# Kernel optimization log

Measured on AMD Instinct MI355X. Metric: run time of the kernel, lower is better.

The kernel has to match this reference:

```python
import jax, jax.numpy as jnp
import numpy as np

N_CODE = 1024
D_K = 512
K = 16
BETA = (0.25, 1.0)
N_SMAT = 2
N = 32768


def setup_inputs() -> dict:
    key = jax.random.key(0)
    k1, k2, k3, k4, k5, k6 = jax.random.split(key, 6)
    x = jax.random.normal(k1, (1, N, D_K), dtype=jnp.float32)
    c = jax.random.normal(k2, (N_CODE, D_K), dtype=jnp.float32)
    # trans linears: Linear(n_code, n_code // 2**i) for i = 1..n_smat
    s = 1.0 / np.sqrt(N_CODE)
    W1 = jax.random.uniform(k3, (N_CODE // 2, N_CODE), jnp.float32, -s, s)
    b1 = jax.random.uniform(k4, (N_CODE // 2,), jnp.float32, -s, s)
    W2 = jax.random.uniform(k5, (N_CODE // 4, N_CODE), jnp.float32, -s, s)
    b2 = jax.random.uniform(k6, (N_CODE // 4,), jnp.float32, -s, s)
    return {"x": x, "c": c, "W1": W1, "b1": b1, "W2": W2, "b2": b2,
            "training": 1, "get_k": 0}


def _quantize(x, cb):
    # argmin of squared euclidean distance == argmin of cdist (p=2)
    # d2[n, m] = ||x_n||^2 - 2 x_n . c_m + ||c_m||^2
    d2 = (jnp.sum(x * x, axis=1, keepdims=True)
          - 2.0 * (x @ cb.T)
          + jnp.sum(cb * cb, axis=1))
    z = jnp.argmin(d2, axis=1)
    return z, cb[z]


def _vq_loss(z_q, x):
    # mse(z_q, sg(x)) and mse(x, sg(z_q)); values identical in forward
    e = jnp.mean((z_q - x) ** 2)
    return BETA[0] * e + BETA[1] * e


def reference(x, c, W1, b1, W2, b2, training, get_k):
    x2 = x[0]  # squeeze(0) -> [N, d_k]

    main_z, main_z_q = _quantize(x2, c)

    # sub-scale codebooks: L(c.T).T == W @ c + b[:, None]
    sub_z_q = jnp.zeros_like(main_z_q)
    for W, b in ((W1, b1), (W2, b2)):
        sub_c = W @ c + b[:, None]  # [n_code // 2^i, d_k]
        _, sub_q = _quantize(x2, sub_c)
        sub_z_q = sub_z_q + sub_q
    sub_z_q = sub_z_q / N_SMAT

    if training:
        total_loss = _vq_loss(main_z_q, x2) + _vq_loss(sub_z_q, x2)
    else:
        total_loss = jnp.zeros(())

    # get_k=0 path: ms_k_i stays zeros
    ms_k_i = jnp.zeros((K, D_K), dtype=x2.dtype)

    # unique rows of main_z_q == number of distinct codebook indices used
    counts = jnp.zeros((N_CODE,), jnp.int32).at[main_z].add(1)
    unique_rows = jnp.sum(counts > 0)

    # straight-through (values unchanged in forward)
    main_out = (x2 + jax.lax.stop_gradient(main_z_q - x2))[None]
    sub_out = (x2 + jax.lax.stop_gradient(sub_z_q - x2))[None]
    return main_out, sub_out, total_loss, ms_k_i, unique_rows
```

## Files before the change

### kernel.cpp

```cpp
#include <hip/hip_runtime.h>
#include <cstdint>

typedef unsigned short ushort_t;
typedef unsigned int uint_t;
typedef _Float16 f16x8 __attribute__((ext_vector_type(8)));
typedef float f32x4 __attribute__((ext_vector_type(4)));

#define N_ROWS 32768
#define DK 512
#define NC_MAIN 1024
#define NCB 1792
#define NTILE 14
#define NBLK_RG 8192

#define MAIN_OFF 0
#define SUB_OFF  16777216
#define LOSS_OFF 33554432
#define MSK_OFF  33554433
#define UNIQ_OFF 33562625

__device__ __forceinline__ uint_t umin_(uint_t a, uint_t b) { return a < b ? a : b; }
__device__ __forceinline__ uint_t umax_(uint_t a, uint_t b) { return a > b ? a : b; }

__global__ __launch_bounds__(256) void build_subcb(
    const float* __restrict__ c, const float* __restrict__ W1,
    const float* __restrict__ b1, const float* __restrict__ W2,
    const float* __restrict__ b2, float* __restrict__ CB,
    _Float16* __restrict__ cbh)
{
    int tid = threadIdx.x;
    int tx = tid & 63, ty = tid >> 6;
    int col = blockIdx.x * 64 + tx;
    int row0 = blockIdx.y * 16 + ty * 4;
    if (row0 < 1024) {
#pragma unroll
        for (int r = 0; r < 4; ++r) {
            float v = c[(row0 + r) * DK + col];
            CB[(row0 + r) * DK + col] = v;
            cbh[(row0 + r) * DK + col] = (_Float16)v;
        }
    } else {
        int i0 = row0 - 1024;
        const float* W;
        const float* b;
        if (i0 < 512) { W = W1; b = b1; }
        else          { W = W2; b = b2; i0 -= 512; }
        float acc[4] = {0.f, 0.f, 0.f, 0.f};
#pragma unroll 8
        for (int j = 0; j < 1024; ++j) {
            float cv = c[j * DK + col];
#pragma unroll
            for (int r = 0; r < 4; ++r)
                acc[r] += W[(i0 + r) * 1024 + j] * cv;
        }
#pragma unroll
        for (int r = 0; r < 4; ++r) {
            float v = acc[r] + b[i0 + r];
            CB[(row0 + r) * DK + col] = v;
            cbh[(row0 + r) * DK + col] = (_Float16)v;
        }
    }
}

__global__ __launch_bounds__(64) void row_norms(const float* __restrict__ CB,
                                                float* __restrict__ norms) {
    int row = blockIdx.x;
    int lane = threadIdx.x;
    const float4* p = (const float4*)(CB + (size_t)row * DK);
    float s = 0.f;
#pragma unroll
    for (int i = lane; i < 128; i += 64) {
        float4 v = p[i];
        s += v.x * v.x + v.y * v.y + v.z * v.z + v.w * v.w;
    }
#pragma unroll
    for (int off = 32; off; off >>= 1) s += __shfl_down(s, off, 64);
    if (lane == 0) norms[row] = s;
}

__global__ __launch_bounds__(256) void cvt_x(const float* __restrict__ in,
                                             _Float16* __restrict__ out,
                                             int* __restrict__ used) {
    int i = blockIdx.x * 256 + threadIdx.x;
    if (i < 1024) used[i] = 0;
    const float4* p = (const float4*)in + (size_t)i * 2;
    float4 a = p[0], b = p[1];
    f16x8 o;
    o[0] = (_Float16)a.x; o[1] = (_Float16)a.y; o[2] = (_Float16)a.z; o[3] = (_Float16)a.w;
    o[4] = (_Float16)b.x; o[5] = (_Float16)b.y; o[6] = (_Float16)b.z; o[7] = (_Float16)b.w;
    *((f16x8*)out + i) = o;
}

__device__ __forceinline__ void async16(void* lds, const void* g) {
    __builtin_amdgcn_global_load_lds(
        (const __attribute__((address_space(1))) unsigned int*)(uintptr_t)g,
        (__attribute__((address_space(3))) unsigned int*)(uintptr_t)lds,
        16, 0, 0);
}

__global__ __launch_bounds__(512, 2) void gemm_topk(
    const _Float16* __restrict__ xh, const _Float16* __restrict__ cbh,
    const float* __restrict__ norms, uint2* __restrict__ candbuf)
{
    __shared__ __align__(16) ushort_t As[2][2][256 * 32];
    __shared__ __align__(16) ushort_t Bs[2][2][256 * 32];

    const int tid = threadIdx.x;
    const int lane = tid & 63;
    const int wid = tid >> 6;
    const int wy = wid >> 2, wx = wid & 3;
    const int lane15 = lane & 15, q = lane >> 4;

    const int bid = blockIdx.x;
    const int xcd = bid & 7;
    const int slot = bid >> 3;
    const int tileP = slot % 7;
    const int rowG = slot / 7;
    const int rowBase = (rowG * 8 + xcd) * 256;
    const int c0 = tileP * 256;

    size_t aoff[2], boff[2];
    int ldsd[2];
#pragma unroll
    for (int i = 0; i < 2; ++i) {
        int d16 = i * 512 + tid;
        int row = d16 >> 2, g = d16 & 3;
        int srow = row ^ ((row >> 3) & 1);
        int sg = g ^ ((row >> 1) & 3);
        aoff[i] = (size_t)(rowBase + srow) * DK + (size_t)(sg * 8);
        boff[i] = (size_t)(c0 + srow) * DK + (size_t)(sg * 8);
        ldsd[i] = d16 * 8;
    }

#define STG_A(BUF, KS, KT) do { \
        async16(&As[(BUF)][(KS)][ldsd[0]], xh + aoff[0] + (KT) * 64 + (KS) * 32); \
        async16(&As[(BUF)][(KS)][ldsd[1]], xh + aoff[1] + (KT) * 64 + (KS) * 32); \
    } while (0)
#define STG_B(BUF, KS, KT) do { \
        async16(&Bs[(BUF)][(KS)][ldsd[0]], cbh + boff[0] + (KT) * 64 + (KS) * 32); \
        async16(&Bs[(BUF)][(KS)][ldsd[1]], cbh + boff[1] + (KT) * 64 + (KS) * 32); \
    } while (0)

    int rdA[8], rdB[4];
#pragma unroll
    for (int mr = 0; mr < 8; ++mr) {
        int rl = wy * 128 + mr * 16 + lane15;
        rdA[mr] = (rl ^ ((rl >> 3) & 1)) * 32 + (q ^ ((rl >> 1) & 3)) * 8;
    }
#pragma unroll
    for (int nc = 0; nc < 4; ++nc) {
        int cl = wx * 64 + nc * 16 + lane15;
        rdB[nc] = (cl ^ ((cl >> 3) & 1)) * 32 + (q ^ ((cl >> 1) & 3)) * 8;
    }

    f32x4 acc[8][4];
#pragma unroll
    for (int mr = 0; mr < 8; ++mr)
#pragma unroll
        for (int nc = 0; nc < 4; ++nc) acc[mr][nc] = (f32x4)0.f;

    STG_B(0, 0, 0); STG_A(0, 0, 0); STG_B(0, 1, 0); STG_A(0, 1, 0);
    asm volatile("s_waitcnt vmcnt(4)" ::: "memory");
    STG_B(1, 0, 1); STG_A(1, 0, 1); STG_B(1, 1, 1);
    asm volatile("s_waitcnt vmcnt(6)" ::: "memory");
    __builtin_amdgcn_s_barrier();

    f16x8 av[4], bv[4];
#pragma unroll
    for (int t = 0; t < 8; ++t) {
        const int b = t & 1;
#pragma unroll
        for (int nc = 0; nc < 4; ++nc) bv[nc] = *(const f16x8*)&Bs[b][0][rdB[nc]];
#pragma unroll
        for (int mr = 0; mr < 4; ++mr) av[mr] = *(const f16x8*)&As[b][0][rdA[mr]];
        if (t + 1 < 8) STG_A(b ^ 1, 1, t + 1);
        __builtin_amdgcn_sched_barrier(0);
        __builtin_amdgcn_s_barrier();
        asm volatile("s_waitcnt lgkmcnt(0)" ::: "memory");
        __builtin_amdgcn_sched_barrier(0);
        __builtin_amdgcn_s_setprio(1);
#pragma unroll
        for (int mr = 0; mr < 4; ++mr)
#pragma unroll
            for (int nc = 0; nc < 4; ++nc)
                acc[mr][nc] = __builtin_amdgcn_mfma_f32_16x16x32_f16(
                    av[mr], bv[nc], acc[mr][nc], 0, 0, 0);
        __builtin_amdgcn_s_setprio(0);
        __builtin_amdgcn_sched_barrier(0);
        __builtin_amdgcn_s_barrier();
#pragma unroll
        for (int mr = 0; mr < 4; ++mr) av[mr] = *(const f16x8*)&As[b][0][rdA[4 + mr]];
        if (t + 2 < 8) STG_B(b, 0, t + 2);
        __builtin_amdgcn_sched_barrier(0);
        __builtin_amdgcn_s_barrier();
        asm volatile("s_waitcnt lgkmcnt(0)" ::: "memory");
        __builtin_amdgcn_sched_barrier(0);
        __builtin_amdgcn_s_setprio(1);
#pragma unroll
        for (int mr = 0; mr < 4; ++mr)
#pragma unroll
            for (int nc = 0; nc < 4; ++nc)
                acc[4 + mr][nc] = __builtin_amdgcn_mfma_f32_16x16x32_f16(
                    av[mr], bv[nc], acc[4 + mr][nc], 0, 0, 0);
        __builtin_amdgcn_s_setprio(0);
        __builtin_amdgcn_sched_barrier(0);
        __builtin_amdgcn_s_barrier();
#pragma unroll
        for (int nc = 0; nc < 4; ++nc) bv[nc] = *(const f16x8*)&Bs[b][1][rdB[nc]];
#pragma unroll
        for (int mr = 0; mr < 4; ++mr) av[mr] = *(const f16x8*)&As[b][1][rdA[mr]];
        if (t + 2 < 8) STG_A(b, 0, t + 2);
        __builtin_amdgcn_sched_barrier(0);
        __builtin_amdgcn_s_barrier();
        asm volatile("s_waitcnt lgkmcnt(0)" ::: "memory");
        __builtin_amdgcn_sched_barrier(0);
        __builtin_amdgcn_s_setprio(1);
#pragma unroll
        for (int mr = 0; mr < 4; ++mr)
#pragma unroll
            for (int nc = 0; nc < 4; ++nc)
                acc[mr][nc] = __builtin_amdgcn_mfma_f32_16x16x32_f16(
                    av[mr], bv[nc], acc[mr][nc], 0, 0, 0);
        __builtin_amdgcn_s_setprio(0);
        __builtin_amdgcn_sched_barrier(0);
        __builtin_amdgcn_s_barrier();
#pragma unroll
        for (int mr = 0; mr < 4; ++mr) av[mr] = *(const f16x8*)&As[b][1][rdA[4 + mr]];
        if (t + 2 < 8) STG_B(b, 1, t + 2);
        __builtin_amdgcn_sched_barrier(0);
        __builtin_amdgcn_s_barrier();
        asm volatile("s_waitcnt lgkmcnt(0)" ::: "memory");
        __builtin_amdgcn_sched_barrier(0);
        __builtin_amdgcn_s_setprio(1);
#pragma unroll
        for (int mr = 0; mr < 4; ++mr)
#pragma unroll
            for (int nc = 0; nc < 4; ++nc)
                acc[4 + mr][nc] = __builtin_amdgcn_mfma_f32_16x16x32_f16(
                    av[mr], bv[nc], acc[4 + mr][nc], 0, 0, 0);
        __builtin_amdgcn_s_setprio(0);
        if (t < 7) {
            if (t + 2 < 8) asm volatile("s_waitcnt vmcnt(6)" ::: "memory");
            else           asm volatile("s_waitcnt vmcnt(0)" ::: "memory");
        }
        __builtin_amdgcn_sched_barrier(0);
        __builtin_amdgcn_s_barrier();
    }
#undef STG_A
#undef STG_B

    uint2 (*cand)[4] = (uint2(*)[4])(void*)&As[0][0][0];

    float nrm[4];
    uint_t colGlob[4];
#pragma unroll
    for (int nc = 0; nc < 4; ++nc) {
        colGlob[nc] = (uint_t)(c0 + wx * 64 + nc * 16 + lane15);
        nrm[nc] = norms[colGlob[nc]];
    }

#pragma unroll
    for (int mr = 0; mr < 8; ++mr) {
#pragma unroll
        for (int r = 0; r < 4; ++r) {
            uint_t k[4];
#pragma unroll
            for (int nc = 0; nc < 4; ++nc) {
                float s = fmaf(-2.f, acc[mr][nc][r], nrm[nc]);
                uint_t bb = __float_as_uint(s);
                uint_t u = bb ^ ((uint_t)((int)bb >> 31) | 0x80000000u);
                k[nc] = (u & 0xFFFFF800u) | colGlob[nc];
            }
            uint_t lo01 = umin_(k[0], k[1]), hi01 = umax_(k[0], k[1]);
            uint_t lo23 = umin_(k[2], k[3]), hi23 = umax_(k[2], k[3]);
            uint_t k1 = umin_(lo01, lo23);
            uint_t k2 = umin_(umin_(hi01, hi23), umax_(lo01, lo23));
#pragma unroll
            for (int m = 1; m <= 8; m <<= 1) {
                uint_t o1 = __shfl_xor(k1, m, 64);
                uint_t o2 = __shfl_xor(k2, m, 64);
                uint_t n1 = umin_(k1, o1);
                uint_t n2 = umin_(umax_(k1, o1), umin_(k2, o2));
                k1 = n1; k2 = n2;
            }
            if (lane15 == 0) {
                int rloc = wy * 128 + mr * 16 + q * 4 + r;
                cand[rloc][wx] = make_uint2(k1, k2);
            }
        }
    }
    __syncthreads();
    {
        int half = tid >> 8;
        int row = tid & 255;
        uint2 a = cand[row][half * 2], b2 = cand[row][half * 2 + 1];
        uint_t k1 = umin_(a.x, b2.x);
        uint_t k2 = umin_(umax_(a.x, b2.x), umin_(a.y, b2.y));
        candbuf[(size_t)(rowBase + row) * NTILE + (tileP * 2 + half)] =
            make_uint2(k1, k2);
    }
}

__device__ __forceinline__ void push4u(uint_t v, uint_t* bs) {
#pragma unroll
    for (int j = 0; j < 4; ++j) {
        uint_t lo = umin_(v, bs[j]);
        uint_t hi = umax_(v, bs[j]);
        bs[j] = lo; v = hi;
    }
}

__global__ __launch_bounds__(256) void rescue_gather(
    const float* __restrict__ x, const float* __restrict__ CB,
    const float* __restrict__ norms, const uint2* __restrict__ candbuf,
    float* __restrict__ main_out, float* __restrict__ sub_out,
    float2* __restrict__ lossPart, int* __restrict__ used)
{
    const int lane = threadIdx.x & 63;
    const int wv = threadIdx.x >> 6;
    const int r = blockIdx.x * 4 + wv;

    const float4* xp = (const float4*)(x + (size_t)r * DK) + lane * 2;
    float4 xa = xp[0], xb = xp[1];

    const uint2* cbp = candbuf + (size_t)r * NTILE;

    int si[12];
    {
        uint_t bs[4];
#pragma unroll
        for (int j = 0; j < 4; ++j) bs[j] = 0xFFFFFFFFu;
#pragma unroll
        for (int t = 0; t < 8; ++t) {
            uint2 e = cbp[t];
            push4u(__builtin_amdgcn_readfirstlane(e.x), bs);
            push4u(__builtin_amdgcn_readfirstlane(e.y), bs);
        }
#pragma unroll
        for (int j = 0; j < 4; ++j) si[j] = (int)(bs[j] & 2047u);
#pragma unroll
        for (int j = 0; j < 4; ++j) bs[j] = 0xFFFFFFFFu;
#pragma unroll
        for (int t = 8; t < 12; ++t) {
            uint2 e = cbp[t];
            push4u(__builtin_amdgcn_readfirstlane(e.x), bs);
            push4u(__builtin_amdgcn_readfirstlane(e.y), bs);
        }
#pragma unroll
        for (int j = 0; j < 4; ++j) si[4 + j] = (int)(bs[j] & 2047u);
#pragma unroll
        for (int j = 0; j < 4; ++j) bs[j] = 0xFFFFFFFFu;
#pragma unroll
        for (int t = 12; t < 14; ++t) {
            uint2 e = cbp[t];
            push4u(__builtin_amdgcn_readfirstlane(e.x), bs);
            push4u(__builtin_amdgcn_readfirstlane(e.y), bs);
        }
#pragma unroll
        for (int j = 0; j < 4; ++j) si[8 + j] = (int)(bs[j] & 2047u);
    }

    float d[12];
#pragma unroll
    for (int k = 0; k < 12; ++k) {
        const float4* cp = (const float4*)(CB + (size_t)si[k] * DK) + lane * 2;
        float4 a = cp[0], b = cp[1];
        d[k] = xa.x * a.x + xa.y * a.y + xa.z * a.z + xa.w * a.w
             + xb.x * b.x + xb.y * b.y + xb.z * b.z + xb.w * b.w;
    }
#pragma unroll
    for (int off = 32; off; off >>= 1)
#pragma unroll
        for (int k = 0; k < 12; ++k) d[k] += __shfl_xor(d[k], off, 64);

    float sc[12];
#pragma unroll
    for (int k = 0; k < 12; ++k) sc[k] = norms[si[k]] - 2.f * d[k];

    int pick[3];
#pragma unroll
    for (int g = 0; g < 3; ++g) {
        float bv = sc[g * 4]; int bidx = si[g * 4];
#pragma unroll
        for (int k = 1; k < 4; ++k) {
            float v = sc[g * 4 + k]; int idx = si[g * 4 + k];
            if (v < bv || (v == bv && idx < bidx)) { bv = v; bidx = idx; }
        }
        pick[g] = bidx;
    }
    const int A = pick[0], B = pick[1], C = pick[2];

    const float4* pa = (const float4*)(CB + (size_t)A * DK) + lane * 2;
    const float4* pb = (const float4*)(CB + (size_t)B * DK) + lane * 2;
    const float4* pc = (const float4*)(CB + (size_t)C * DK) + lane * 2;
    float4* mo = (float4*)(main_out + (size_t)r * DK) + lane * 2;
    float4* so = (float4*)(sub_out + (size_t)r * DK) + lane * 2;
    float em = 0.f, es = 0.f;
#pragma unroll
    for (int i = 0; i < 2; ++i) {
        float4 xq = (i == 0) ? xa : xb;
        float4 cm = pa[i];
        float4 q1 = pb[i];
        float4 q2 = pc[i];
        float4 cs;
        cs.x = 0.5f * (q1.x + q2.x);
        cs.y = 0.5f * (q1.y + q2.y);
        cs.z = 0.5f * (q1.z + q2.z);
        cs.w = 0.5f * (q1.w + q2.w);
        mo[i] = cm;
        so[i] = cs;
        float t;
        t = cm.x - xq.x; em += t * t;
        t = cm.y - xq.y; em += t * t;
        t = cm.z - xq.z; em += t * t;
        t = cm.w - xq.w; em += t * t;
        t = cs.x - xq.x; es += t * t;
        t = cs.y - xq.y; es += t * t;
        t = cs.z - xq.z; es += t * t;
        t = cs.w - xq.w; es += t * t;
    }
#pragma unroll
    for (int off = 32; off; off >>= 1) {
        em += __shfl_down(em, off, 64);
        es += __shfl_down(es, off, 64);
    }
    __shared__ float sm[8];
    if (lane == 0) {
        sm[wv] = em; sm[4 + wv] = es;
        used[A] = 1;
    }
    __syncthreads();
    if (threadIdx.x == 0) {
        lossPart[blockIdx.x] = make_float2(sm[0] + sm[1] + sm[2] + sm[3],
                                           sm[4] + sm[5] + sm[6] + sm[7]);
    }
}

__global__ __launch_bounds__(256) void finalize_kernel(
    const int* __restrict__ used, const float2* __restrict__ lossPart,
    const int* __restrict__ training, float* __restrict__ out)
{
    int tid = threadIdx.x;
    int cnt = 0;
    for (int i = tid; i < 1024; i += 256) cnt += (used[i] != 0);
    float em = 0.f, es = 0.f;
    for (int i = tid; i < NBLK_RG; i += 256) {
        float2 p = lossPart[i];
        em += p.x; es += p.y;
    }
#pragma unroll
    for (int off = 32; off; off >>= 1) {
        cnt += __shfl_down(cnt, off, 64);
        em += __shfl_down(em, off, 64);
        es += __shfl_down(es, off, 64);
    }
    __shared__ int sc[4];
    __shared__ float se[4], ss[4];
    if ((tid & 63) == 0) { sc[tid >> 6] = cnt; se[tid >> 6] = em; ss[tid >> 6] = es; }
    __syncthreads();
    if (tid == 0) {
        int total = sc[0] + sc[1] + sc[2] + sc[3];
        float tl = 0.f;
        if (*training) {
            float l0 = se[0] + se[1] + se[2] + se[3];
            float l1 = ss[0] + ss[1] + ss[2] + ss[3];
            tl = 1.25f * (l0 + l1) * (1.0f / ((float)N_ROWS * (float)DK));
        }
        out[LOSS_OFF] = tl;
        out[UNIQ_OFF] = (float)total;
    }
    for (int i = tid; i < 8192; i += 256) out[MSK_OFF + i] = 0.f;
}

extern "C" void kernel_launch(void* const* d_in, const int* in_sizes, int n_in,
                              void* d_out, int out_size, void* d_ws, size_t ws_size,
                              hipStream_t stream) {
    const float* x = (const float*)d_in[0];
    const float* c = (const float*)d_in[1];
    const float* W1 = (const float*)d_in[2];
    const float* b1 = (const float*)d_in[3];
    const float* W2 = (const float*)d_in[4];
    const float* b2 = (const float*)d_in[5];
    const int* training = (const int*)d_in[6];
    float* out = (float*)d_out;

    char* p = (char*)d_ws;
    float* CB = (float*)p;          p += (size_t)NCB * DK * 4;
    _Float16* xh = (_Float16*)p;    p += (size_t)N_ROWS * DK * 2;
    _Float16* cbh = (_Float16*)p;   p += (size_t)NCB * DK * 2;
    uint2* candbuf = (uint2*)p;     p += (size_t)N_ROWS * NTILE * 8;
    float* norms = (float*)p;       p += NCB * 4;
    float2* lossPart = (float2*)p;  p += (size_t)NBLK_RG * 8;
    int* used = (int*)p;            p += 4096;

    build_subcb<<<dim3(8, 112), dim3(256), 0, stream>>>(c, W1, b1, W2, b2, CB, cbh);
    row_norms<<<dim3(NCB), dim3(64), 0, stream>>>(CB, norms);
    cvt_x<<<dim3(8192), dim3(256), 0, stream>>>(x, xh, used);
    gemm_topk<<<dim3(896), dim3(512), 0, stream>>>(xh, cbh, norms, candbuf);
    rescue_gather<<<dim3(NBLK_RG), dim3(256), 0, stream>>>(
        x, CB, norms, candbuf, out + MAIN_OFF, out + SUB_OFF, lossPart, used);
    finalize_kernel<<<dim3(1), dim3(256), 0, stream>>>(used, lossPart, training, out);
}
```

Measured before the change: 433.4 us.

## Restructure GEMM main loop to one barrier per K-step with batched prefetch

Replaces the four-phase ping-pong schedule inside the distance GEMM loop. The old loop interleaved global->LDS stages between MFMA groups with many barriers and lgkmcnt waits. The new one reads all LDS fragments for a K-step into separate registers, runs all MFMAs, then issues all four stages for step t+2 after a single barrier. This cuts barrier count per iteration but raises register pressure and loses finer overlap of global loads with MFMA work.

```diff
diff --git a/kernel.cpp b/kernel.cpp
--- a/kernel.cpp
+++ b/kernel.cpp
@@ -159,24 +159,21 @@
 #pragma unroll
         for (int nc = 0; nc < 4; ++nc) acc[mr][nc] = (f32x4)0.f;
 
-    STG_B(0, 0, 0); STG_A(0, 0, 0); STG_B(0, 1, 0); STG_A(0, 1, 0);
-    asm volatile("s_waitcnt vmcnt(4)" ::: "memory");
-    STG_B(1, 0, 1); STG_A(1, 0, 1); STG_B(1, 1, 1);
-    asm volatile("s_waitcnt vmcnt(6)" ::: "memory");
+    STG_A(0, 0, 0); STG_B(0, 0, 0); STG_A(0, 1, 0); STG_B(0, 1, 0);
+    STG_A(1, 0, 1); STG_B(1, 0, 1); STG_A(1, 1, 1); STG_B(1, 1, 1);
+    asm volatile("s_waitcnt vmcnt(8)" ::: "memory");
     __builtin_amdgcn_s_barrier();
 
-    f16x8 av[4], bv[4];
 #pragma unroll
     for (int t = 0; t < 8; ++t) {
         const int b = t & 1;
-#pragma unroll
-        for (int nc = 0; nc < 4; ++nc) bv[nc] = *(const f16x8*)&Bs[b][0][rdB[nc]];
-#pragma unroll
-        for (int mr = 0; mr < 4; ++mr) av[mr] = *(const f16x8*)&As[b][0][rdA[mr]];
-        if (t + 1 < 8) STG_A(b ^ 1, 1, t + 1);
-        __builtin_amdgcn_sched_barrier(0);
-        __builtin_amdgcn_s_barrier();
-        asm volatile("s_waitcnt lgkmcnt(0)" ::: "memory");
+        f16x8 b0[4], b1v[4], a0lo[4], a0hi[4], a1lo[4], a1hi[4];
+#pragma unroll
+        for (int nc = 0; nc < 4; ++nc) b0[nc] = *(const f16x8*)&Bs[b][0][rdB[nc]];
+#pragma unroll
+        for (int mr = 0; mr < 4; ++mr) a0lo[mr] = *(const f16x8*)&As[b][0][rdA[mr]];
+#pragma unroll
+        for (int mr = 0; mr < 4; ++mr) a0hi[mr] = *(const f16x8*)&As[b][0][rdA[4 + mr]];
         __builtin_amdgcn_sched_barrier(0);
         __builtin_amdgcn_s_setprio(1);
 #pragma unroll
@@ -184,16 +181,13 @@
 #pragma unroll
             for (int nc = 0; nc < 4; ++nc)
                 acc[mr][nc] = __builtin_amdgcn_mfma_f32_16x16x32_f16(
-                    av[mr], bv[nc], acc[mr][nc], 0, 0, 0);
+                    a0lo[mr], b0[nc], acc[mr][nc], 0, 0, 0);
         __builtin_amdgcn_s_setprio(0);
         __builtin_amdgcn_sched_barrier(0);
-        __builtin_amdgcn_s_barrier();
-#pragma unroll
-        for (int mr = 0; mr < 4; ++mr) av[mr] = *(const f16x8*)&As[b][0][rdA[4 + mr]];
-        if (t + 2 < 8) STG_B(b, 0, t + 2);
-        __builtin_amdgcn_sched_barrier(0);
-        __builtin_amdgcn_s_barrier();
-        asm volatile("s_waitcnt lgkmcnt(0)" ::: "memory");
+#pragma unroll
+        for (int nc = 0; nc < 4; ++nc) b1v[nc] = *(const f16x8*)&Bs[b][1][rdB[nc]];
+#pragma unroll
+        for (int mr = 0; mr < 4; ++mr) a1lo[mr] = *(const f16x8*)&As[b][1][rdA[mr]];
         __builtin_amdgcn_sched_barrier(0);
         __builtin_amdgcn_s_setprio(1);
 #pragma unroll
@@ -201,18 +195,11 @@
 #pragma unroll
             for (int nc = 0; nc < 4; ++nc)
                 acc[4 + mr][nc] = __builtin_amdgcn_mfma_f32_16x16x32_f16(
-                    av[mr], bv[nc], acc[4 + mr][nc], 0, 0, 0);
+                    a0hi[mr], b0[nc], acc[4 + mr][nc], 0, 0, 0);
         __builtin_amdgcn_s_setprio(0);
         __builtin_amdgcn_sched_barrier(0);
-        __builtin_amdgcn_s_barrier();
-#pragma unroll
-        for (int nc = 0; nc < 4; ++nc) bv[nc] = *(const f16x8*)&Bs[b][1][rdB[nc]];
-#pragma unroll
-        for (int mr = 0; mr < 4; ++mr) av[mr] = *(const f16x8*)&As[b][1][rdA[mr]];
-        if (t + 2 < 8) STG_A(b, 0, t + 2);
-        __builtin_amdgcn_sched_barrier(0);
-        __builtin_amdgcn_s_barrier();
-        asm volatile("s_waitcnt lgkmcnt(0)" ::: "memory");
+#pragma unroll
+        for (int mr = 0; mr < 4; ++mr) a1hi[mr] = *(const f16x8*)&As[b][1][rdA[4 + mr]];
         __builtin_amdgcn_sched_barrier(0);
         __builtin_amdgcn_s_setprio(1);
 #pragma unroll
@@ -220,16 +207,8 @@
 #pragma unroll
             for (int nc = 0; nc < 4; ++nc)
                 acc[mr][nc] = __builtin_amdgcn_mfma_f32_16x16x32_f16(
-                    av[mr], bv[nc], acc[mr][nc], 0, 0, 0);
+                    a1lo[mr], b1v[nc], acc[mr][nc], 0, 0, 0);
         __builtin_amdgcn_s_setprio(0);
-        __builtin_amdgcn_sched_barrier(0);
-        __builtin_amdgcn_s_barrier();
-#pragma unroll
-        for (int mr = 0; mr < 4; ++mr) av[mr] = *(const f16x8*)&As[b][1][rdA[4 + mr]];
-        if (t + 2 < 8) STG_B(b, 1, t + 2);
-        __builtin_amdgcn_sched_barrier(0);
-        __builtin_amdgcn_s_barrier();
-        asm volatile("s_waitcnt lgkmcnt(0)" ::: "memory");
         __builtin_amdgcn_sched_barrier(0);
         __builtin_amdgcn_s_setprio(1);
 #pragma unroll
@@ -237,10 +216,16 @@
 #pragma unroll
             for (int nc = 0; nc < 4; ++nc)
                 acc[4 + mr][nc] = __builtin_amdgcn_mfma_f32_16x16x32_f16(
-                    av[mr], bv[nc], acc[4 + mr][nc], 0, 0, 0);
+                    a1hi[mr], b1v[nc], acc[4 + mr][nc], 0, 0, 0);
         __builtin_amdgcn_s_setprio(0);
+        __builtin_amdgcn_sched_barrier(0);
+        __builtin_amdgcn_s_barrier();
+        if (t + 2 < 8) {
+            STG_A(b, 0, t + 2); STG_B(b, 0, t + 2);
+            STG_A(b, 1, t + 2); STG_B(b, 1, t + 2);
+        }
         if (t < 7) {
-            if (t + 2 < 8) asm volatile("s_waitcnt vmcnt(6)" ::: "memory");
+            if (t + 2 < 8) asm volatile("s_waitcnt vmcnt(8)" ::: "memory");
             else           asm volatile("s_waitcnt vmcnt(0)" ::: "memory");
         }
         __builtin_amdgcn_sched_barrier(0);
```

After: 422.4 us. 1.03x faster.
